# Performance work log

Hardware: AMD Instinct MI355X
Metric: run time of the kernel (lower is better)

Reference implementation:

```python
import jax, jax.numpy as jnp
import numpy as np

N_NODES = 10000
N_EDGES = 160000
NUM_FEAT = 14
DIM = 256


def gat_conv(x, src, dst, W, a_s, a_d, b, concat):
    """PyG GATConv: W [H*C, F_in], a_s/a_d [H, C], edges src->dst (self-loops included)."""
    H, C = a_s.shape
    N = x.shape[0]
    h = (x @ W.T).reshape(N, H, C)                       # [N,H,C]
    alpha_src = (h * a_s).sum(-1)                        # [N,H]
    alpha_dst = (h * a_d).sum(-1)                        # [N,H]
    e = jax.nn.leaky_relu(alpha_src[src] + alpha_dst[dst], negative_slope=0.2)  # [E,H]
    emax = jax.ops.segment_max(e, dst, num_segments=N)   # [N,H]
    emax = jnp.where(jnp.isneginf(emax), 0.0, emax)
    ex = jnp.exp(e - emax[dst])
    denom = jax.ops.segment_sum(ex, dst, num_segments=N)
    coef = ex / (denom[dst] + 1e-16)                     # segment softmax over in-edges
    out = jax.ops.segment_sum(h[src] * coef[..., None], dst, num_segments=N)  # [N,H,C]
    out = out.reshape(N, H * C) if concat else out.mean(axis=1)
    return out + b


def setup_inputs() -> dict:
    key = jax.random.key(0)
    ks = jax.random.split(key, 24)
    d = DIM
    f = NUM_FEAT
    def w(k, shape, fan_in):
        return jax.random.normal(k, shape, dtype=jnp.float32) * (1.0 / np.sqrt(fan_in))
    inp = {
        "x": jax.random.normal(ks[0], (N_NODES, f), dtype=jnp.float32),
        "edge_index": jax.random.randint(ks[1], (2, N_EDGES), 0, N_NODES, dtype=jnp.int64
                                         if jax.config.jax_enable_x64 else jnp.int32),
        # conv1: 14 -> 4 heads x 256
        "W1": w(ks[2], (4 * d, f), f),
        "a1s": w(ks[3], (4, d), d), "a1d": w(ks[4], (4, d), d),
        "b1": jnp.zeros((4 * d,), jnp.float32),
        "lw1": w(ks[5], (4 * d, f), f), "lb1": jnp.zeros((4 * d,), jnp.float32),
        # conv2: 1024 -> 4 heads x 256
        "W2": w(ks[6], (4 * d, 4 * d), 4 * d),
        "a2s": w(ks[7], (4, d), d), "a2d": w(ks[8], (4, d), d),
        "b2": jnp.zeros((4 * d,), jnp.float32),
        "lw2": w(ks[9], (4 * d, 4 * d), 4 * d), "lb2": jnp.zeros((4 * d,), jnp.float32),
        # conv3: 1024 -> 6 heads x 256, mean over heads
        "W3": w(ks[10], (6 * d, 4 * d), 4 * d),
        "a3s": w(ks[11], (6, d), d), "a3d": w(ks[12], (6, d), d),
        "b3": jnp.zeros((d,), jnp.float32),
        "lw3": w(ks[13], (d, 4 * d), 4 * d), "lb3": jnp.zeros((d,), jnp.float32),
    }
    return inp


def reference(x, edge_index, W1, a1s, a1d, b1, lw1, lb1,
              W2, a2s, a2d, b2, lw2, lb2,
              W3, a3s, a3d, b3, lw3, lb3):
    N = x.shape[0]
    loops = jnp.arange(N, dtype=edge_index.dtype)
    src = jnp.concatenate([edge_index[0], loops])
    dst = jnp.concatenate([edge_index[1], loops])
    x1 = jax.nn.elu(gat_conv(x, src, dst, W1, a1s, a1d, b1, True) + x @ lw1.T + lb1)
    x2 = jax.nn.elu(gat_conv(x1, src, dst, W2, a2s, a2d, b2, True) + x1 @ lw2.T + lb2)
    x3 = gat_conv(x2, src, dst, W3, a3s, a3d, b3, False) + x2 @ lw3.T + lb3
    return x3
```

## Files before the change

### kernel.cpp

```cpp
#include <hip/hip_runtime.h>
#include <hip/hip_bf16.h>
#include <cstddef>

#define NN 10000
#define EE0 160000
#define NF 14
#define DC 256

static inline int ceildiv(int a, int b) { return (a + b - 1) / b; }

__device__ __forceinline__ float lrelu02(float x) { return fmaxf(x, 0.2f * x); }

__device__ __forceinline__ short f2bf(float f) {
    unsigned u = __float_as_uint(f);
    unsigned r = (u + 0x7FFFu + ((u >> 16) & 1u)) >> 16;
    return (short)r;
}
__device__ __forceinline__ float bf2f(short s) {
    return __uint_as_float(((unsigned)(unsigned short)s) << 16);
}

typedef __attribute__((ext_vector_type(8))) short bf16x8;
typedef __attribute__((ext_vector_type(4))) float f32x4;

#define GLDS(gaddr, laddr)                                                         \
    __builtin_amdgcn_global_load_lds(                                              \
        (__attribute__((address_space(1))) void*)(gaddr),                          \
        (__attribute__((address_space(3))) void*)(laddr), 16, 0, 0)

__global__ void count_edges_k(const int* __restrict__ ei, int* __restrict__ counts,
                              int E0, int N) {
    int e = blockIdx.x * 256 + threadIdx.x;
    int E = E0 + N;
    if (e >= E) return;
    int dst = (e < E0) ? ei[E0 + e] : (e - E0);
    atomicAdd(&counts[dst], 1);
}

__global__ __launch_bounds__(1024) void scan_k(const int* __restrict__ counts,
                                               int* __restrict__ row_off, int n) {
    __shared__ int sums[1024];
    int t = threadIdx.x;
    int chunk = (n + 1023) >> 10;
    int base = t * chunk;
    int lim = base + chunk; if (lim > n) lim = n;
    int s = 0;
    for (int i = base; i < lim; ++i) s += counts[i];
    sums[t] = s;
    __syncthreads();
    for (int off = 1; off < 1024; off <<= 1) {
        int v = (t >= off) ? sums[t - off] : 0;
        __syncthreads();
        sums[t] += v;
        __syncthreads();
    }
    int run = (t == 0) ? 0 : sums[t - 1];
    for (int i = base; i < lim; ++i) { run += counts[i]; row_off[i + 1] = run; }
    if (t == 0) row_off[0] = 0;
}

__global__ void scatter_k(const int* __restrict__ ei, const int* __restrict__ row_off,
                          int* __restrict__ cursor, int* __restrict__ csr_src,
                          int E0, int N) {
    int e = blockIdx.x * 256 + threadIdx.x;
    int E = E0 + N;
    if (e >= E) return;
    int src, dst;
    if (e < E0) { src = ei[e]; dst = ei[E0 + e]; }
    else        { src = dst = e - E0; }
    int pos = row_off[dst] + atomicAdd(&cursor[dst], 1);
    csr_src[pos] = src;
}

__global__ __launch_bounds__(256) void cvt_bf16_fused_k(
    const float* __restrict__ p0, short* __restrict__ q0, int n0,
    const float* __restrict__ p1, short* __restrict__ q1, int n1,
    const float* __restrict__ p2, short* __restrict__ q2, int n2,
    const float* __restrict__ p3, short* __restrict__ q3, int n3) {
    int i = blockIdx.x * 256 + threadIdx.x;
    const float* in; short* out; int idx;
    if (i < n0) { in = p0; out = q0; idx = i; }
    else if (i < n0 + n1) { in = p1; out = q1; idx = i - n0; }
    else if (i < n0 + n1 + n2) { in = p2; out = q2; idx = i - n0 - n1; }
    else if (i < n0 + n1 + n2 + n3) { in = p3; out = q3; idx = i - n0 - n1 - n2; }
    else return;
    float4 v = ((const float4*)in)[idx];
    short4 o;
    o.x = f2bf(v.x); o.y = f2bf(v.y); o.z = f2bf(v.z); o.w = f2bf(v.w);
    ((short4*)out)[idx] = o;
}

__global__ __launch_bounds__(256) void pad_bf16_k(
    const float* __restrict__ p0, short* __restrict__ q0, int r0,
    const float* __restrict__ p1, short* __restrict__ q1, int r1,
    const float* __restrict__ p2, short* __restrict__ q2, int r2,
    int K, int Kp) {
    int i = blockIdx.x * 256 + threadIdx.x;
    int rows = r0 + r1 + r2;
    int total = rows * Kp;
    if (i >= total) return;
    int row = i / Kp, col = i - row * Kp;
    const float* in; short* out; int r;
    if (row < r0) { in = p0; out = q0; r = row; }
    else if (row < r0 + r1) { in = p1; out = q1; r = row - r0; }
    else { in = p2; out = q2; r = row - r0 - r1; }
    out[(size_t)r * Kp + col] = (col < K) ? f2bf(in[(size_t)r * K + col]) : (short)0;
}

__global__ __launch_bounds__(256) void gemm_bf16_dual(
    const short* __restrict__ A, const short* __restrict__ B,
    const float* __restrict__ b1, const float* __restrict__ b2,
    short* __restrict__ Cb, float* __restrict__ Cf,
    int M, int Nh, int Nf, int K) {
    __shared__ short As[128 * 32];
    __shared__ short Bs[128 * 32];
    const int t = threadIdx.x;
    const int wave = t >> 6, lane = t & 63;
    const int m0 = blockIdx.y * 128, n0 = blockIdx.x * 128;
    const int wm = (wave >> 1) * 64, wn = (wave & 1) * 64;
    const int lane15 = lane & 15, quad = lane >> 4;

    const int lrow = lane >> 2;
    const int lk = ((lane & 3) ^ ((lrow >> 1) & 3)) * 8;
    int arow0 = m0 + wave * 16 + lrow;
    int arow1 = arow0 + 64;
    if (arow0 > M - 1) arow0 = M - 1;
    if (arow1 > M - 1) arow1 = M - 1;
    const short* ag0 = A + (size_t)arow0 * K + lk;
    const short* ag1 = A + (size_t)arow1 * K + lk;
    const short* bg0 = B + (size_t)(n0 + wave * 16 + lrow) * K + lk;
    const short* bg1 = B + (size_t)(n0 + 64 + wave * 16 + lrow) * K + lk;
    short* al0 = &As[(wave * 16) * 32];
    short* al1 = &As[(64 + wave * 16) * 32];
    short* bl0 = &Bs[(wave * 16) * 32];
    short* bl1 = &Bs[(64 + wave * 16) * 32];

    const int rql = (quad ^ ((lane15 >> 1) & 3)) * 8;

    f32x4 acc[4][4];
#pragma unroll
    for (int i = 0; i < 4; ++i)
#pragma unroll
        for (int j = 0; j < 4; ++j) acc[i][j] = (f32x4){0.f, 0.f, 0.f, 0.f};

    for (int k0 = 0; k0 < K; k0 += 32) {
        GLDS(ag0 + k0, al0);
        GLDS(ag1 + k0, al1);
        GLDS(bg0 + k0, bl0);
        GLDS(bg1 + k0, bl1);
        __syncthreads();
        bf16x8 af[4], bfr[4];
#pragma unroll
        for (int i = 0; i < 4; ++i)
            af[i] = *(const bf16x8*)&As[(wm + 16 * i + lane15) * 32 + rql];
#pragma unroll
        for (int j = 0; j < 4; ++j)
            bfr[j] = *(const bf16x8*)&Bs[(wn + 16 * j + lane15) * 32 + rql];
#pragma unroll
        for (int i = 0; i < 4; ++i)
#pragma unroll
            for (int j = 0; j < 4; ++j)
                acc[i][j] = __builtin_amdgcn_mfma_f32_16x16x32_bf16(
                    af[i], bfr[j], acc[i][j], 0, 0, 0);
        __syncthreads();
    }

    if (n0 >= Nh) {
#pragma unroll
        for (int j = 0; j < 4; ++j) {
            int nc = n0 - Nh + wn + 16 * j + lane15;
            float bias = b1[nc] + b2[nc];
#pragma unroll
            for (int i = 0; i < 4; ++i) {
                int mb = m0 + wm + 16 * i + quad * 4;
#pragma unroll
                for (int r = 0; r < 4; ++r) {
                    int m = mb + r;
                    if (m < M) Cf[(size_t)m * Nf + nc] = acc[i][j][r] + bias;
                }
            }
        }
    } else {
#pragma unroll
        for (int j = 0; j < 4; ++j) {
            int n = n0 + wn + 16 * j + lane15;
#pragma unroll
            for (int i = 0; i < 4; ++i) {
                int mb = m0 + wm + 16 * i + quad * 4;
#pragma unroll
                for (int r = 0; r < 4; ++r) {
                    int m = mb + r;
                    if (m < M) Cb[(size_t)m * Nh + n] = f2bf(acc[i][j][r]);
                }
            }
        }
    }
}

__global__ __launch_bounds__(256) void alpha_k(
    const short* __restrict__ h, const float* __restrict__ a_s,
    const float* __restrict__ a_d, float* __restrict__ asrc,
    float* __restrict__ adst, int N, int H) {
    int wid = (int)((blockIdx.x * (size_t)blockDim.x + threadIdx.x) >> 6);
    int lane = threadIdx.x & 63;
    if (wid >= N * H) return;
    int n = wid / H, hh = wid - n * H;
    const short4 hv4 = *(const short4*)(h + (size_t)n * H * DC + hh * DC + lane * 4);
    const float4 sv = *(const float4*)(a_s + hh * DC + lane * 4);
    const float4 dv = *(const float4*)(a_d + hh * DC + lane * 4);
    float hx = bf2f(hv4.x), hy = bf2f(hv4.y), hz = bf2f(hv4.z), hw = bf2f(hv4.w);
    float s = hx * sv.x + hy * sv.y + hz * sv.z + hw * sv.w;
    float d = hx * dv.x + hy * dv.y + hz * dv.z + hw * dv.w;
#pragma unroll
    for (int off = 32; off > 0; off >>= 1) {
        s += __shfl_down(s, off);
        d += __shfl_down(d, off);
    }
    if (lane == 0) { asrc[wid] = s; adst[wid] = d; }
}

__global__ __launch_bounds__(256) void gat_agg(
    const short* __restrict__ hbuf, const float* __restrict__ lin,
    const float* __restrict__ asrc, const float* __restrict__ adst_a,
    const int* __restrict__ row_off, const int* __restrict__ csr_src,
    short* __restrict__ outx, int N, int H) {
    int wid = (int)((blockIdx.x * (size_t)blockDim.x + threadIdx.x) >> 6);
    int lane = threadIdx.x & 63;
    if (wid >= N * H) return;
    int n = wid / H, hh = wid - n * H;
    int beg = row_off[n], end = row_off[n + 1];
    int deg = end - beg;
    float ad = adst_a[wid];

    size_t cbase = (size_t)n * H * DC + hh * DC + lane * 4;
    float4 acc = *(const float4*)(lin + cbase);

    if (deg <= 64) {
        int s = 0; float e = -1e38f;
        if (lane < deg) {
            s = csr_src[beg + lane];
            e = lrelu02(asrc[s * H + hh] + ad);
        }
        float m = e;
#pragma unroll
        for (int off = 32; off > 0; off >>= 1) m = fmaxf(m, __shfl_xor(m, off));
        float p = (lane < deg) ? __expf(e - m) : 0.f;
        float dsum = p;
#pragma unroll
        for (int off = 32; off > 0; off >>= 1) dsum += __shfl_xor(dsum, off);
        float coef = p / (dsum + 1e-16f);

        const size_t hoff = (size_t)hh * DC + lane * 4;
        int i = 0;
        for (; i + 8 <= deg; i += 8) {
            short4 v[8]; float wv[8];
#pragma unroll
            for (int u = 0; u < 8; ++u) {
                int su = __shfl(s, i + u);
                v[u] = *(const short4*)(hbuf + (size_t)su * (H * DC) + hoff);
                wv[u] = __shfl(coef, i + u);
            }
#pragma unroll
            for (int u = 0; u < 8; ++u) {
                acc.x += wv[u] * bf2f(v[u].x);
                acc.y += wv[u] * bf2f(v[u].y);
                acc.z += wv[u] * bf2f(v[u].z);
                acc.w += wv[u] * bf2f(v[u].w);
            }
        }
        for (; i < deg; ++i) {
            float wv = __shfl(coef, i);
            int si = __shfl(s, i);
            const short4 hv = *(const short4*)(hbuf + (size_t)si * (H * DC) + hoff);
            acc.x += wv * bf2f(hv.x); acc.y += wv * bf2f(hv.y);
            acc.z += wv * bf2f(hv.z); acc.w += wv * bf2f(hv.w);
        }
    } else {
        float m = -1e38f;
        for (int i = beg + lane; i < end; i += 64) {
            int s = csr_src[i];
            m = fmaxf(m, lrelu02(asrc[s * H + hh] + ad));
        }
#pragma unroll
        for (int off = 32; off > 0; off >>= 1) m = fmaxf(m, __shfl_xor(m, off));
        float dsum = 0.f;
        for (int i = beg + lane; i < end; i += 64) {
            int s = csr_src[i];
            dsum += __expf(lrelu02(asrc[s * H + hh] + ad) - m);
        }
#pragma unroll
        for (int off = 32; off > 0; off >>= 1) dsum += __shfl_xor(dsum, off);
        float inv = 1.f / (dsum + 1e-16f);
        for (int i = beg; i < end; ++i) {
            int s = csr_src[i];
            float wv = __expf(lrelu02(asrc[s * H + hh] + ad) - m) * inv;
            const short4 hv = *(const short4*)(hbuf + ((size_t)s * H + hh) * DC + lane * 4);
            acc.x += wv * bf2f(hv.x); acc.y += wv * bf2f(hv.y);
            acc.z += wv * bf2f(hv.z); acc.w += wv * bf2f(hv.w);
        }
    }
    acc.x = acc.x > 0.f ? acc.x : __expf(acc.x) - 1.f;
    acc.y = acc.y > 0.f ? acc.y : __expf(acc.y) - 1.f;
    acc.z = acc.z > 0.f ? acc.z : __expf(acc.z) - 1.f;
    acc.w = acc.w > 0.f ? acc.w : __expf(acc.w) - 1.f;
    short4 o;
    o.x = f2bf(acc.x); o.y = f2bf(acc.y); o.z = f2bf(acc.z); o.w = f2bf(acc.w);
    *(short4*)(outx + cbase) = o;
}

__global__ __launch_bounds__(256) void gat_agg_mean(
    const short* __restrict__ hbuf, const float* __restrict__ asrc,
    const float* __restrict__ adst_a, const int* __restrict__ row_off,
    const int* __restrict__ csr_src, float* __restrict__ out, int N) {
    const int H = 6;
    int wid = (int)((blockIdx.x * (size_t)blockDim.x + threadIdx.x) >> 6);
    int lane = threadIdx.x & 63;
    if (wid >= N) return;
    int n = wid;
    int beg = row_off[n], end = row_off[n + 1];
    int deg = end - beg;
    const float invH = 1.f / 6.f;

    float4 acc = *(const float4*)(out + (size_t)n * DC + lane * 4);

    if (deg <= 64) {
        int s = 0;
        float as6[6];
        if (lane < deg) {
            s = csr_src[beg + lane];
            const float2* ap = (const float2*)(asrc + (size_t)s * H);
            float2 v0 = ap[0], v1 = ap[1], v2 = ap[2];
            as6[0] = v0.x; as6[1] = v0.y; as6[2] = v1.x;
            as6[3] = v1.y; as6[4] = v2.x; as6[5] = v2.y;
        }
        float coefh[6];
#pragma unroll
        for (int hh = 0; hh < 6; ++hh) {
            float ad = adst_a[n * H + hh];
            float e = (lane < deg) ? lrelu02(as6[hh] + ad) : -1e38f;
            float m = e;
#pragma unroll
            for (int off = 32; off > 0; off >>= 1) m = fmaxf(m, __shfl_xor(m, off));
            float p = (lane < deg) ? __expf(e - m) : 0.f;
            float dsum = p;
#pragma unroll
            for (int off = 32; off > 0; off >>= 1) dsum += __shfl_xor(dsum, off);
            coefh[hh] = p * invH / (dsum + 1e-16f);
        }
        int i = 0;
        for (; i + 2 <= deg; i += 2) {
            int sa = __shfl(s, i), sb = __shfl(s, i + 1);
            const short* ha = hbuf + (size_t)sa * (H * DC) + lane * 4;
            const short* hb = hbuf + (size_t)sb * (H * DC) + lane * 4;
            short4 va[6], vb[6];
#pragma unroll
            for (int hh = 0; hh < 6; ++hh) {
                va[hh] = *(const short4*)(ha + hh * DC);
                vb[hh] = *(const short4*)(hb + hh * DC);
            }
#pragma unroll
            for (int hh = 0; hh < 6; ++hh) {
                float wa = __shfl(coefh[hh], i), wb = __shfl(coefh[hh], i + 1);
                acc.x += wa * bf2f(va[hh].x) + wb * bf2f(vb[hh].x);
                acc.y += wa * bf2f(va[hh].y) + wb * bf2f(vb[hh].y);
                acc.z += wa * bf2f(va[hh].z) + wb * bf2f(vb[hh].z);
                acc.w += wa * bf2f(va[hh].w) + wb * bf2f(vb[hh].w);
            }
        }
        if (i < deg) {
            int si = __shfl(s, i);
            const short* hb = hbuf + (size_t)si * (H * DC) + lane * 4;
#pragma unroll
            for (int hh = 0; hh < 6; ++hh) {
                float wv = __shfl(coefh[hh], i);
                const short4 hv = *(const short4*)(hb + hh * DC);
                acc.x += wv * bf2f(hv.x); acc.y += wv * bf2f(hv.y);
                acc.z += wv * bf2f(hv.z); acc.w += wv * bf2f(hv.w);
            }
        }
    } else {
        for (int hh = 0; hh < 6; ++hh) {
            float ad = adst_a[n * H + hh];
            float m = -1e38f;
            for (int i = beg + lane; i < end; i += 64) {
                int s = csr_src[i];
                m = fmaxf(m, lrelu02(asrc[s * H + hh] + ad));
            }
#pragma unroll
            for (int off = 32; off > 0; off >>= 1) m = fmaxf(m, __shfl_xor(m, off));
            float dsum = 0.f;
            for (int i = beg + lane; i < end; i += 64) {
                int s = csr_src[i];
                dsum += __expf(lrelu02(asrc[s * H + hh] + ad) - m);
            }
#pragma unroll
            for (int off = 32; off > 0; off >>= 1) dsum += __shfl_xor(dsum, off);
            float inv = invH / (dsum + 1e-16f);
            for (int i = beg; i < end; ++i) {
                int s = csr_src[i];
                float wv = __expf(lrelu02(asrc[s * H + hh] + ad) - m) * inv;
                const short4 hv =
                    *(const short4*)(hbuf + (size_t)s * (H * DC) + hh * DC + lane * 4);
                acc.x += wv * bf2f(hv.x); acc.y += wv * bf2f(hv.y);
                acc.z += wv * bf2f(hv.z); acc.w += wv * bf2f(hv.w);
            }
        }
    }
    *(float4*)(out + (size_t)n * DC + lane * 4) = acc;
}

extern "C" void kernel_launch(void* const* d_in, const int* in_sizes, int n_in,
                              void* d_out, int out_size, void* d_ws, size_t ws_size,
                              hipStream_t stream) {
    const float* x   = (const float*)d_in[0];
    const int*   ei  = (const int*)d_in[1];
    const float* W1  = (const float*)d_in[2];
    const float* a1s = (const float*)d_in[3];
    const float* a1d = (const float*)d_in[4];
    const float* b1  = (const float*)d_in[5];
    const float* lw1 = (const float*)d_in[6];
    const float* lb1 = (const float*)d_in[7];
    const float* W2  = (const float*)d_in[8];
    const float* a2s = (const float*)d_in[9];
    const float* a2d = (const float*)d_in[10];
    const float* b2  = (const float*)d_in[11];
    const float* lw2 = (const float*)d_in[12];
    const float* lb2 = (const float*)d_in[13];
    const float* W3  = (const float*)d_in[14];
    const float* a3s = (const float*)d_in[15];
    const float* a3d = (const float*)d_in[16];
    const float* b3  = (const float*)d_in[17];
    const float* lw3 = (const float*)d_in[18];
    const float* lb3 = (const float*)d_in[19];
    float* out = (float*)d_out;

    const int N = NN, E0 = EE0, E = EE0 + NN;

    unsigned char* w = (unsigned char*)d_ws;
    size_t off = 0;
    auto alloc = [&](size_t bytes) {
        void* p = w + off;
        off += (bytes + 255) & ~(size_t)255;
        return p;
    };
    short* hbuf   = (short*)alloc((size_t)N * 1536 * 2);
    float* buf    = (float*)alloc((size_t)N * 1024 * 4);
    short* xb     = (short*)alloc((size_t)N * 1024 * 2);
    short* xpad   = (short*)alloc((size_t)N * 32 * 2);
    short* W1p    = (short*)alloc((size_t)1024 * 32 * 2);
    short* lw1p   = (short*)alloc((size_t)1024 * 32 * 2);
    short* W2b    = (short*)alloc((size_t)1024 * 1024 * 2);
    short* lw2b   = (short*)alloc((size_t)1024 * 1024 * 2);
    short* W3b    = (short*)alloc((size_t)1536 * 1024 * 2);
    short* lw3b   = (short*)alloc((size_t)256 * 1024 * 2);
    float* asrc   = (float*)alloc((size_t)N * 6 * 4);
    float* adst   = (float*)alloc((size_t)N * 6 * 4);
    int* row_off  = (int*)alloc((size_t)(N + 1) * 4);
    int* counts2  = (int*)alloc((size_t)2 * N * 4);
    int* counts   = counts2;
    int* cursor   = counts2 + N;
    int* csr_src  = (int*)alloc((size_t)E * 4);
    (void)ws_size; (void)n_in; (void)in_sizes; (void)out_size;

    hipMemsetAsync(counts2, 0, (size_t)2 * N * 4, stream);
    count_edges_k<<<ceildiv(E, 256), 256, 0, stream>>>(ei, counts, E0, N);
    scan_k<<<1, 1024, 0, stream>>>(counts, row_off, N);
    scatter_k<<<ceildiv(E, 256), 256, 0, stream>>>(ei, row_off, cursor, csr_src, E0, N);

    {
        int q0 = 1024 * 1024 / 4, q1 = 1024 * 1024 / 4, q2 = 1536 * 1024 / 4,
            q3 = 256 * 1024 / 4;
        cvt_bf16_fused_k<<<ceildiv(q0 + q1 + q2 + q3, 256), 256, 0, stream>>>(
            W2, W2b, q0, lw2, lw2b, q1, W3, W3b, q2, lw3, lw3b, q3);
        int rows = N + 1024 + 1024;
        pad_bf16_k<<<ceildiv(rows * 32, 256), 256, 0, stream>>>(
            x, xpad, N, W1, W1p, 1024, lw1, lw1p, 1024, NF, 32);
    }

    gemm_bf16_dual<<<dim3(16, ceildiv(N, 128)), 256, 0, stream>>>(
        xpad, W1p, b1, lb1, hbuf, buf, N, 1024, 1024, 32);
    alpha_k<<<ceildiv(N * 4, 4), 256, 0, stream>>>(hbuf, a1s, a1d, asrc, adst, N, 4);
    gat_agg<<<ceildiv(N * 4, 4), 256, 0, stream>>>(hbuf, buf, asrc, adst, row_off, csr_src,
                                                   xb, N, 4);

    gemm_bf16_dual<<<dim3(16, ceildiv(N, 128)), 256, 0, stream>>>(
        xb, W2b, b2, lb2, hbuf, buf, N, 1024, 1024, 1024);
    alpha_k<<<ceildiv(N * 4, 4), 256, 0, stream>>>(hbuf, a2s, a2d, asrc, adst, N, 4);
    gat_agg<<<ceildiv(N * 4, 4), 256, 0, stream>>>(hbuf, buf, asrc, adst, row_off, csr_src,
                                                   xb, N, 4);

    gemm_bf16_dual<<<dim3(14, ceildiv(N, 128)), 256, 0, stream>>>(
        xb, W3b, b3, lb3, hbuf, out, N, 1536, 256, 1024);
    alpha_k<<<ceildiv(N * 6, 4), 256, 0, stream>>>(hbuf, a3s, a3d, asrc, adst, N, 6);
    gat_agg_mean<<<ceildiv(N, 4), 256, 0, stream>>>(hbuf, asrc, adst, row_off, csr_src,
                                                    out, N);
}
```

Measured before the change: 490.3 us.

## Aggregate two heads per wavefront with 16-byte bf16x8 gathers

The GAT aggregation kernels now have each wavefront cover two heads (512 channels). Each lane gathers 8 bf16 values with one 16-byte load instead of 4 values with an 8-byte load, which halves the number of gather instructions and wavefronts. Each half-wave now computes the softmax for its own head, so the short-degree path drops from 64 to 32 neighbours and more nodes take the slower high-degree path. The mean kernel applies the same layout, combines the two halves with a cross-half shuffle, and its high-degree path now reads each neighbour row once for all heads instead of once per head.

```diff
diff --git a/kernel.cpp b/kernel.cpp
--- a/kernel.cpp
+++ b/kernel.cpp
@@ -219,93 +219,100 @@
     if (lane == 0) { asrc[wid] = s; adst[wid] = d; }
 }
 
-__global__ __launch_bounds__(256) void gat_agg(
+__global__ __launch_bounds__(256) void gat_agg_pair(
     const short* __restrict__ hbuf, const float* __restrict__ lin,
     const float* __restrict__ asrc, const float* __restrict__ adst_a,
     const int* __restrict__ row_off, const int* __restrict__ csr_src,
     short* __restrict__ outx, int N, int H) {
+    const int npair = H >> 1;
     int wid = (int)((blockIdx.x * (size_t)blockDim.x + threadIdx.x) >> 6);
     int lane = threadIdx.x & 63;
-    if (wid >= N * H) return;
-    int n = wid / H, hh = wid - n * H;
+    if (wid >= N * npair) return;
+    int n = wid / npair, p = wid - n * npair;
     int beg = row_off[n], end = row_off[n + 1];
     int deg = end - beg;
-    float ad = adst_a[wid];
-
-    size_t cbase = (size_t)n * H * DC + hh * DC + lane * 4;
-    float4 acc = *(const float4*)(lin + cbase);
-
-    if (deg <= 64) {
+    int half = lane >> 5, sub = lane & 31;
+    int head = 2 * p + half;
+    float ad = adst_a[n * H + head];
+
+    const size_t cbase = (size_t)n * (H * DC) + p * 512 + lane * 8;
+    float acc[8];
+    {
+        const float* lp = lin + cbase;
+        float4 l0 = *(const float4*)lp;
+        float4 l1 = *(const float4*)(lp + 4);
+        acc[0] = l0.x; acc[1] = l0.y; acc[2] = l0.z; acc[3] = l0.w;
+        acc[4] = l1.x; acc[5] = l1.y; acc[6] = l1.z; acc[7] = l1.w;
+    }
+
+    if (deg <= 32) {
         int s = 0; float e = -1e38f;
-        if (lane < deg) {
-            s = csr_src[beg + lane];
-            e = lrelu02(asrc[s * H + hh] + ad);
+        if (sub < deg) {
+            s = csr_src[beg + sub];
+            e = lrelu02(asrc[s * H + head] + ad);
         }
         float m = e;
 #pragma unroll
-        for (int off = 32; off > 0; off >>= 1) m = fmaxf(m, __shfl_xor(m, off));
-        float p = (lane < deg) ? __expf(e - m) : 0.f;
-        float dsum = p;
-#pragma unroll
-        for (int off = 32; off > 0; off >>= 1) dsum += __shfl_xor(dsum, off);
-        float coef = p / (dsum + 1e-16f);
-
-        const size_t hoff = (size_t)hh * DC + lane * 4;
+        for (int off = 16; off > 0; off >>= 1) m = fmaxf(m, __shfl_xor(m, off));
+        float pr = (sub < deg) ? __expf(e - m) : 0.f;
+        float ds = pr;
+#pragma unroll
+        for (int off = 16; off > 0; off >>= 1) ds += __shfl_xor(ds, off);
+        float coef = pr / (ds + 1e-16f);
+
         int i = 0;
-        for (; i + 8 <= deg; i += 8) {
-            short4 v[8]; float wv[8];
-#pragma unroll
-            for (int u = 0; u < 8; ++u) {
+        for (; i + 4 <= deg; i += 4) {
+            bf16x8 v[4]; float wv[4];
+#pragma unroll
+            for (int u = 0; u < 4; ++u) {
                 int su = __shfl(s, i + u);
-                v[u] = *(const short4*)(hbuf + (size_t)su * (H * DC) + hoff);
-                wv[u] = __shfl(coef, i + u);
-            }
-#pragma unroll
-            for (int u = 0; u < 8; ++u) {
-                acc.x += wv[u] * bf2f(v[u].x);
-                acc.y += wv[u] * bf2f(v[u].y);
-                acc.z += wv[u] * bf2f(v[u].z);
-                acc.w += wv[u] * bf2f(v[u].w);
-            }
+                v[u] = *(const bf16x8*)(hbuf + (size_t)su * (H * DC) + p * 512 + lane * 8);
+                wv[u] = __shfl(coef, (half << 5) + i + u);
+            }
+#pragma unroll
+            for (int u = 0; u < 4; ++u)
+#pragma unroll
+                for (int c = 0; c < 8; ++c) acc[c] += wv[u] * bf2f(v[u][c]);
         }
         for (; i < deg; ++i) {
-            float wv = __shfl(coef, i);
-            int si = __shfl(s, i);
-            const short4 hv = *(const short4*)(hbuf + (size_t)si * (H * DC) + hoff);
-            acc.x += wv * bf2f(hv.x); acc.y += wv * bf2f(hv.y);
-            acc.z += wv * bf2f(hv.z); acc.w += wv * bf2f(hv.w);
+            int su = __shfl(s, i);
+            float wv = __shfl(coef, (half << 5) + i);
+            bf16x8 v = *(const bf16x8*)(hbuf + (size_t)su * (H * DC) + p * 512 + lane * 8);
+#pragma unroll
+            for (int c = 0; c < 8; ++c) acc[c] += wv * bf2f(v[c]);
         }
     } else {
         float m = -1e38f;
-        for (int i = beg + lane; i < end; i += 64) {
+        for (int i = beg + sub; i < end; i += 32) {
             int s = csr_src[i];
-            m = fmaxf(m, lrelu02(asrc[s * H + hh] + ad));
-        }
-#pragma unroll
-        for (int off = 32; off > 0; off >>= 1) m = fmaxf(m, __shfl_xor(m, off));
-        float dsum = 0.f;
-        for (int i = beg + lane; i < end; i += 64) {
+            m = fmaxf(m, lrelu02(asrc[s * H + head] + ad));
+        }
+#pragma unroll
+        for (int off = 16; off > 0; off >>= 1) m = fmaxf(m, __shfl_xor(m, off));
+        float ds = 0.f;
+        for (int i = beg + sub; i < end; i += 32) {
             int s = csr_src[i];
-            dsum += __expf(lrelu02(asrc[s * H + hh] + ad) - m);
-        }
-#pragma unroll
-        for (int off = 32; off > 0; off >>= 1) dsum += __shfl_xor(dsum, off);
-        float inv = 1.f / (dsum + 1e-16f);
+            ds += __expf(lrelu02(asrc[s * H + head] + ad) - m);
+        }
+#pragma unroll
+        for (int off = 16; off > 0; off >>= 1) ds += __shfl_xor(ds, off);
+        float inv = 1.f / (ds + 1e-16f);
         for (int i = beg; i < end; ++i) {
             int s = csr_src[i];
-            float wv = __expf(lrelu02(asrc[s * H + hh] + ad) - m) * inv;
-            const short4 hv = *(const short4*)(hbuf + ((size_t)s * H + hh) * DC + lane * 4);
-            acc.x += wv * bf2f(hv.x); acc.y += wv * bf2f(hv.y);
-            acc.z += wv * bf2f(hv.z); acc.w += wv * bf2f(hv.w);
-        }
-    }
-    acc.x = acc.x > 0.f ? acc.x : __expf(acc.x) - 1.f;
-    acc.y = acc.y > 0.f ? acc.y : __expf(acc.y) - 1.f;
-    acc.z = acc.z > 0.f ? acc.z : __expf(acc.z) - 1.f;
-    acc.w = acc.w > 0.f ? acc.w : __expf(acc.w) - 1.f;
-    short4 o;
-    o.x = f2bf(acc.x); o.y = f2bf(acc.y); o.z = f2bf(acc.z); o.w = f2bf(acc.w);
-    *(short4*)(outx + cbase) = o;
+            float wv = __expf(lrelu02(asrc[s * H + head] + ad) - m) * inv;
+            bf16x8 v = *(const bf16x8*)(hbuf + (size_t)s * (H * DC) + p * 512 + lane * 8);
+#pragma unroll
+            for (int c = 0; c < 8; ++c) acc[c] += wv * bf2f(v[c]);
+        }
+    }
+    bf16x8 o;
+#pragma unroll
+    for (int c = 0; c < 8; ++c) {
+        float a = acc[c];
+        a = a > 0.f ? a : __expf(a) - 1.f;
+        o[c] = f2bf(a);
+    }
+    *(bf16x8*)(outx + cbase) = o;
 }
 
 __global__ __launch_bounds__(256) void gat_agg_mean(
@@ -319,9 +326,12 @@
     int n = wid;
     int beg = row_off[n], end = row_off[n + 1];
     int deg = end - beg;
+    int half = lane >> 5, sub = lane & 31;
     const float invH = 1.f / 6.f;
 
-    float4 acc = *(const float4*)(out + (size_t)n * DC + lane * 4);
+    float acc[8];
+#pragma unroll
+    for (int c = 0; c < 8; ++c) acc[c] = 0.f;
 
     if (deg <= 64) {
         int s = 0;
@@ -341,72 +351,92 @@
             float m = e;
 #pragma unroll
             for (int off = 32; off > 0; off >>= 1) m = fmaxf(m, __shfl_xor(m, off));
-            float p = (lane < deg) ? __expf(e - m) : 0.f;
-            float dsum = p;
+            float pv = (lane < deg) ? __expf(e - m) : 0.f;
+            float dsum = pv;
 #pragma unroll
             for (int off = 32; off > 0; off >>= 1) dsum += __shfl_xor(dsum, off);
-            coefh[hh] = p * invH / (dsum + 1e-16f);
+            coefh[hh] = pv * invH / (dsum + 1e-16f);
         }
         int i = 0;
         for (; i + 2 <= deg; i += 2) {
             int sa = __shfl(s, i), sb = __shfl(s, i + 1);
-            const short* ha = hbuf + (size_t)sa * (H * DC) + lane * 4;
-            const short* hb = hbuf + (size_t)sb * (H * DC) + lane * 4;
-            short4 va[6], vb[6];
-#pragma unroll
-            for (int hh = 0; hh < 6; ++hh) {
-                va[hh] = *(const short4*)(ha + hh * DC);
-                vb[hh] = *(const short4*)(hb + hh * DC);
-            }
-#pragma unroll
-            for (int hh = 0; hh < 6; ++hh) {
-                float wa = __shfl(coefh[hh], i), wb = __shfl(coefh[hh], i + 1);
-                acc.x += wa * bf2f(va[hh].x) + wb * bf2f(vb[hh].x);
-                acc.y += wa * bf2f(va[hh].y) + wb * bf2f(vb[hh].y);
-                acc.z += wa * bf2f(va[hh].z) + wb * bf2f(vb[hh].z);
-                acc.w += wa * bf2f(va[hh].w) + wb * bf2f(vb[hh].w);
+            const short* ba = hbuf + (size_t)sa * (H * DC) + lane * 8;
+            const short* bb = hbuf + (size_t)sb * (H * DC) + lane * 8;
+            bf16x8 va[3], vb[3];
+#pragma unroll
+            for (int j = 0; j < 3; ++j) {
+                va[j] = *(const bf16x8*)(ba + j * 512);
+                vb[j] = *(const bf16x8*)(bb + j * 512);
+            }
+#pragma unroll
+            for (int j = 0; j < 3; ++j) {
+                float wa0 = __shfl(coefh[2 * j], i), wa1 = __shfl(coefh[2 * j + 1], i);
+                float wb0 = __shfl(coefh[2 * j], i + 1), wb1 = __shfl(coefh[2 * j + 1], i + 1);
+                float wA = half ? wa1 : wa0;
+                float wB = half ? wb1 : wb0;
+#pragma unroll
+                for (int c = 0; c < 8; ++c)
+                    acc[c] += wA * bf2f(va[j][c]) + wB * bf2f(vb[j][c]);
             }
         }
         if (i < deg) {
             int si = __shfl(s, i);
-            const short* hb = hbuf + (size_t)si * (H * DC) + lane * 4;
-#pragma unroll
-            for (int hh = 0; hh < 6; ++hh) {
-                float wv = __shfl(coefh[hh], i);
-                const short4 hv = *(const short4*)(hb + hh * DC);
-                acc.x += wv * bf2f(hv.x); acc.y += wv * bf2f(hv.y);
-                acc.z += wv * bf2f(hv.z); acc.w += wv * bf2f(hv.w);
+            const short* bi = hbuf + (size_t)si * (H * DC) + lane * 8;
+#pragma unroll
+            for (int j = 0; j < 3; ++j) {
+                bf16x8 v = *(const bf16x8*)(bi + j * 512);
+                float w0 = __shfl(coefh[2 * j], i), w1 = __shfl(coefh[2 * j + 1], i);
+                float wv = half ? w1 : w0;
+#pragma unroll
+                for (int c = 0; c < 8; ++c) acc[c] += wv * bf2f(v[c]);
             }
         }
     } else {
+        float m6[6], inv6[6], ad6[6];
+#pragma unroll
+        for (int hh = 0; hh < 6; ++hh) ad6[hh] = adst_a[n * H + hh];
         for (int hh = 0; hh < 6; ++hh) {
-            float ad = adst_a[n * H + hh];
             float m = -1e38f;
             for (int i = beg + lane; i < end; i += 64) {
                 int s = csr_src[i];
-                m = fmaxf(m, lrelu02(asrc[s * H + hh] + ad));
+                m = fmaxf(m, lrelu02(asrc[s * H + hh] + ad6[hh]));
             }
 #pragma unroll
             for (int off = 32; off > 0; off >>= 1) m = fmaxf(m, __shfl_xor(m, off));
-            float dsum = 0.f;
+            float ds = 0.f;
             for (int i = beg + lane; i < end; i += 64) {
                 int s = csr_src[i];
-                dsum += __expf(lrelu02(asrc[s * H + hh] + ad) - m);
-            }
-#pragma unroll
-            for (int off = 32; off > 0; off >>= 1) dsum += __shfl_xor(dsum, off);
-            float inv = invH / (dsum + 1e-16f);
-            for (int i = beg; i < end; ++i) {
-                int s = csr_src[i];
-                float wv = __expf(lrelu02(asrc[s * H + hh] + ad) - m) * inv;
-                const short4 hv =
-                    *(const short4*)(hbuf + (size_t)s * (H * DC) + hh * DC + lane * 4);
-                acc.x += wv * bf2f(hv.x); acc.y += wv * bf2f(hv.y);
-                acc.z += wv * bf2f(hv.z); acc.w += wv * bf2f(hv.w);
-            }
-        }
-    }
-    *(float4*)(out + (size_t)n * DC + lane * 4) = acc;
+                ds += __expf(lrelu02(asrc[s * H + hh] + ad6[hh]) - m);
+            }
+#pragma unroll
+            for (int off = 32; off > 0; off >>= 1) ds += __shfl_xor(ds, off);
+            m6[hh] = m;
+            inv6[hh] = invH / (ds + 1e-16f);
+        }
+        for (int i = beg; i < end; ++i) {
+            int s = csr_src[i];
+            const short* bi = hbuf + (size_t)s * (H * DC) + lane * 8;
+#pragma unroll
+            for (int j = 0; j < 3; ++j) {
+                int h = 2 * j + half;
+                float wv = __expf(lrelu02(asrc[s * H + h] + ad6[h]) - m6[h]) * inv6[h];
+                bf16x8 v = *(const bf16x8*)(bi + j * 512);
+#pragma unroll
+                for (int c = 0; c < 8; ++c) acc[c] += wv * bf2f(v[c]);
+            }
+        }
+    }
+#pragma unroll
+    for (int c = 0; c < 8; ++c) acc[c] += __shfl_xor(acc[c], 32);
+    if (lane < 32) {
+        float* op = out + (size_t)n * DC + sub * 8;
+        float4 o0 = *(float4*)op;
+        float4 o1 = *(float4*)(op + 4);
+        o0.x += acc[0]; o0.y += acc[1]; o0.z += acc[2]; o0.w += acc[3];
+        o1.x += acc[4]; o1.y += acc[5]; o1.z += acc[6]; o1.w += acc[7];
+        *(float4*)op = o0;
+        *(float4*)(op + 4) = o1;
+    }
 }
 
 extern "C" void kernel_launch(void* const* d_in, const int* in_sizes, int n_in,
@@ -480,14 +510,14 @@
     gemm_bf16_dual<<<dim3(16, ceildiv(N, 128)), 256, 0, stream>>>(
         xpad, W1p, b1, lb1, hbuf, buf, N, 1024, 1024, 32);
     alpha_k<<<ceildiv(N * 4, 4), 256, 0, stream>>>(hbuf, a1s, a1d, asrc, adst, N, 4);
-    gat_agg<<<ceildiv(N * 4, 4), 256, 0, stream>>>(hbuf, buf, asrc, adst, row_off, csr_src,
-                                                   xb, N, 4);
+    gat_agg_pair<<<ceildiv(N * 2, 4), 256, 0, stream>>>(hbuf, buf, asrc, adst, row_off,
+                                                        csr_src, xb, N, 4);
 
     gemm_bf16_dual<<<dim3(16, ceildiv(N, 128)), 256, 0, stream>>>(
         xb, W2b, b2, lb2, hbuf, buf, N, 1024, 1024, 1024);
     alpha_k<<<ceildiv(N * 4, 4), 256, 0, stream>>>(hbuf, a2s, a2d, asrc, adst, N, 4);
-    gat_agg<<<ceildiv(N * 4, 4), 256, 0, stream>>>(hbuf, buf, asrc, adst, row_off, csr_src,
-                                                   xb, N, 4);
+    gat_agg_pair<<<ceildiv(N * 2, 4), 256, 0, stream>>>(hbuf, buf, asrc, adst, row_off,
+                                                        csr_src, xb, N, 4);
 
     gemm_bf16_dual<<<dim3(14, ceildiv(N, 128)), 256, 0, stream>>>(
         xb, W3b, b3, lb3, hbuf, out, N, 1536, 256, 1024);
```

After: 505.8 us. 3.2% more time.

## Split final mean aggregation across six waves per node with LDS head reduction

Applied to the files above, without the earlier changes.

Rewrites the layer-3 mean aggregation so each node gets a 384-thread block with one wave per head, in place of one wave handling all six heads serially. Each wave computes its own head's softmax and gathers with an 8-edge unrolled loop to keep more loads in flight; partial sums are combined through shared memory and added to the output by wave 0. The aim is more parallelism and memory-level concurrency in the gather, at the cost of a block barrier, LDS traffic and one extra store pass per node. A cosmetic rename of the lw2 pointer is also included.

```diff
diff --git a/kernel.cpp b/kernel.cpp
--- a/kernel.cpp
+++ b/kernel.cpp
@@ -308,105 +308,98 @@
     *(short4*)(outx + cbase) = o;
 }
 
-__global__ __launch_bounds__(256) void gat_agg_mean(
+__global__ __launch_bounds__(384) void gat_agg_mean(
     const short* __restrict__ hbuf, const float* __restrict__ asrc,
     const float* __restrict__ adst_a, const int* __restrict__ row_off,
     const int* __restrict__ csr_src, float* __restrict__ out, int N) {
     const int H = 6;
-    int wid = (int)((blockIdx.x * (size_t)blockDim.x + threadIdx.x) >> 6);
-    int lane = threadIdx.x & 63;
-    if (wid >= N) return;
-    int n = wid;
+    __shared__ float red[6][DC];
+    int n = blockIdx.x;
+    int wave = threadIdx.x >> 6, lane = threadIdx.x & 63;
+    int hh = wave;
     int beg = row_off[n], end = row_off[n + 1];
     int deg = end - beg;
     const float invH = 1.f / 6.f;
-
-    float4 acc = *(const float4*)(out + (size_t)n * DC + lane * 4);
+    float ad = adst_a[n * H + hh];
+
+    float4 acc = make_float4(0.f, 0.f, 0.f, 0.f);
+    const size_t hoff = (size_t)hh * DC + lane * 4;
 
     if (deg <= 64) {
-        int s = 0;
-        float as6[6];
+        int s = 0; float e = -1e38f;
         if (lane < deg) {
             s = csr_src[beg + lane];
-            const float2* ap = (const float2*)(asrc + (size_t)s * H);
-            float2 v0 = ap[0], v1 = ap[1], v2 = ap[2];
-            as6[0] = v0.x; as6[1] = v0.y; as6[2] = v1.x;
-            as6[3] = v1.y; as6[4] = v2.x; as6[5] = v2.y;
-        }
-        float coefh[6];
-#pragma unroll
-        for (int hh = 0; hh < 6; ++hh) {
-            float ad = adst_a[n * H + hh];
-            float e = (lane < deg) ? lrelu02(as6[hh] + ad) : -1e38f;
-            float m = e;
-#pragma unroll
-            for (int off = 32; off > 0; off >>= 1) m = fmaxf(m, __shfl_xor(m, off));
-            float p = (lane < deg) ? __expf(e - m) : 0.f;
-            float dsum = p;
-#pragma unroll
-            for (int off = 32; off > 0; off >>= 1) dsum += __shfl_xor(dsum, off);
-            coefh[hh] = p * invH / (dsum + 1e-16f);
-        }
+            e = lrelu02(asrc[s * H + hh] + ad);
+        }
+        float m = e;
+#pragma unroll
+        for (int off = 32; off > 0; off >>= 1) m = fmaxf(m, __shfl_xor(m, off));
+        float p = (lane < deg) ? __expf(e - m) : 0.f;
+        float dsum = p;
+#pragma unroll
+        for (int off = 32; off > 0; off >>= 1) dsum += __shfl_xor(dsum, off);
+        float coef = p * invH / (dsum + 1e-16f);
+
         int i = 0;
-        for (; i + 2 <= deg; i += 2) {
-            int sa = __shfl(s, i), sb = __shfl(s, i + 1);
-            const short* ha = hbuf + (size_t)sa * (H * DC) + lane * 4;
-            const short* hb = hbuf + (size_t)sb * (H * DC) + lane * 4;
-            short4 va[6], vb[6];
-#pragma unroll
-            for (int hh = 0; hh < 6; ++hh) {
-                va[hh] = *(const short4*)(ha + hh * DC);
-                vb[hh] = *(const short4*)(hb + hh * DC);
-            }
-#pragma unroll
-            for (int hh = 0; hh < 6; ++hh) {
-                float wa = __shfl(coefh[hh], i), wb = __shfl(coefh[hh], i + 1);
-                acc.x += wa * bf2f(va[hh].x) + wb * bf2f(vb[hh].x);
-                acc.y += wa * bf2f(va[hh].y) + wb * bf2f(vb[hh].y);
-                acc.z += wa * bf2f(va[hh].z) + wb * bf2f(vb[hh].z);
-                acc.w += wa * bf2f(va[hh].w) + wb * bf2f(vb[hh].w);
-            }
-        }
-        if (i < deg) {
+        for (; i + 8 <= deg; i += 8) {
+            short4 v[8]; float wv[8];
+#pragma unroll
+            for (int u = 0; u < 8; ++u) {
+                int su = __shfl(s, i + u);
+                v[u] = *(const short4*)(hbuf + (size_t)su * (H * DC) + hoff);
+                wv[u] = __shfl(coef, i + u);
+            }
+#pragma unroll
+            for (int u = 0; u < 8; ++u) {
+                acc.x += wv[u] * bf2f(v[u].x);
+                acc.y += wv[u] * bf2f(v[u].y);
+                acc.z += wv[u] * bf2f(v[u].z);
+                acc.w += wv[u] * bf2f(v[u].w);
+            }
+        }
+        for (; i < deg; ++i) {
+            float wv = __shfl(coef, i);
             int si = __shfl(s, i);
-            const short* hb = hbuf + (size_t)si * (H * DC) + lane * 4;
-#pragma unroll
-            for (int hh = 0; hh < 6; ++hh) {
-                float wv = __shfl(coefh[hh], i);
-                const short4 hv = *(const short4*)(hb + hh * DC);
-                acc.x += wv * bf2f(hv.x); acc.y += wv * bf2f(hv.y);
-                acc.z += wv * bf2f(hv.z); acc.w += wv * bf2f(hv.w);
-            }
+            const short4 hv = *(const short4*)(hbuf + (size_t)si * (H * DC) + hoff);
+            acc.x += wv * bf2f(hv.x); acc.y += wv * bf2f(hv.y);
+            acc.z += wv * bf2f(hv.z); acc.w += wv * bf2f(hv.w);
         }
     } else {
-        for (int hh = 0; hh < 6; ++hh) {
-            float ad = adst_a[n * H + hh];
-            float m = -1e38f;
-            for (int i = beg + lane; i < end; i += 64) {
-                int s = csr_src[i];
-                m = fmaxf(m, lrelu02(asrc[s * H + hh] + ad));
-            }
-#pragma unroll
-            for (int off = 32; off > 0; off >>= 1) m = fmaxf(m, __shfl_xor(m, off));
-            float dsum = 0.f;
-            for (int i = beg + lane; i < end; i += 64) {
-                int s = csr_src[i];
-                dsum += __expf(lrelu02(asrc[s * H + hh] + ad) - m);
-            }
-#pragma unroll
-            for (int off = 32; off > 0; off >>= 1) dsum += __shfl_xor(dsum, off);
-            float inv = invH / (dsum + 1e-16f);
-            for (int i = beg; i < end; ++i) {
-                int s = csr_src[i];
-                float wv = __expf(lrelu02(asrc[s * H + hh] + ad) - m) * inv;
-                const short4 hv =
-                    *(const short4*)(hbuf + (size_t)s * (H * DC) + hh * DC + lane * 4);
-                acc.x += wv * bf2f(hv.x); acc.y += wv * bf2f(hv.y);
-                acc.z += wv * bf2f(hv.z); acc.w += wv * bf2f(hv.w);
-            }
-        }
-    }
-    *(float4*)(out + (size_t)n * DC + lane * 4) = acc;
+        float m = -1e38f;
+        for (int i = beg + lane; i < end; i += 64) {
+            int s = csr_src[i];
+            m = fmaxf(m, lrelu02(asrc[s * H + hh] + ad));
+        }
+#pragma unroll
+        for (int off = 32; off > 0; off >>= 1) m = fmaxf(m, __shfl_xor(m, off));
+        float dsum = 0.f;
+        for (int i = beg + lane; i < end; i += 64) {
+            int s = csr_src[i];
+            dsum += __expf(lrelu02(asrc[s * H + hh] + ad) - m);
+        }
+#pragma unroll
+        for (int off = 32; off > 0; off >>= 1) dsum += __shfl_xor(dsum, off);
+        float inv = invH / (dsum + 1e-16f);
+        for (int i = beg; i < end; ++i) {
+            int s = csr_src[i];
+            float wv = __expf(lrelu02(asrc[s * H + hh] + ad) - m) * inv;
+            const short4 hv = *(const short4*)(hbuf + (size_t)s * (H * DC) + hoff);
+            acc.x += wv * bf2f(hv.x); acc.y += wv * bf2f(hv.y);
+            acc.z += wv * bf2f(hv.z); acc.w += wv * bf2f(hv.w);
+        }
+    }
+    *(float4*)&red[wave][lane * 4] = acc;
+    __syncthreads();
+    if (wave == 0) {
+        float* op = out + (size_t)n * DC + lane * 4;
+        float4 o = *(float4*)op;
+#pragma unroll
+        for (int j = 0; j < 6; ++j) {
+            float4 r = *(float4*)&red[j][lane * 4];
+            o.x += r.x; o.y += r.y; o.z += r.z; o.w += r.w;
+        }
+        *(float4*)op = o;
+    }
 }
 
 extern "C" void kernel_launch(void* const* d_in, const int* in_sizes, int n_in,
@@ -424,7 +417,7 @@
     const float* a2s = (const float*)d_in[9];
     const float* a2d = (const float*)d_in[10];
     const float* b2  = (const float*)d_in[11];
-    const float* lw2 = (const float*)d_in[12];
+    const float* lb2_w = (const float*)d_in[12];
     const float* lb2 = (const float*)d_in[13];
     const float* W3  = (const float*)d_in[14];
     const float* a3s = (const float*)d_in[15];
@@ -432,6 +425,7 @@
     const float* b3  = (const float*)d_in[17];
     const float* lw3 = (const float*)d_in[18];
     const float* lb3 = (const float*)d_in[19];
+    const float* lw2 = lb2_w;
     float* out = (float*)d_out;
 
     const int N = NN, E0 = EE0, E = EE0 + NN;
@@ -492,6 +486,5 @@
     gemm_bf16_dual<<<dim3(14, ceildiv(N, 128)), 256, 0, stream>>>(
         xb, W3b, b3, lb3, hbuf, out, N, 1536, 256, 1024);
     alpha_k<<<ceildiv(N * 6, 4), 256, 0, stream>>>(hbuf, a3s, a3d, asrc, adst, N, 6);
-    gat_agg_mean<<<ceildiv(N, 4), 256, 0, stream>>>(hbuf, asrc, adst, row_off, csr_src,
-                                                    out, N);
-}
+    gat_agg_mean<<<N, 384, 0, stream>>>(hbuf, asrc, adst, row_off, csr_src, out, N);
+}
```

Result: no change. 482.6 us (-1.6%).
